# Performance work log

Measured on AMD Instinct MI355X. Metric: run time of the kernel, lower is better.

Reference implementation:

```python
import jax, jax.numpy as jnp
import numpy as np

B, S, D = 2, 2048, 2048
H, DK, DV, LD = 16, 128, 128, 64


def setup_inputs() -> dict:
    key = jax.random.key(0)
    ks = jax.random.split(key, 12)
    s = lambda fan_in: 1.0 / np.sqrt(fan_in)
    return {
        "queries": jax.random.normal(ks[0], (B, S, D), jnp.float32),
        "keys": jax.random.normal(ks[1], (B, S, D), jnp.float32),
        "values": jax.random.normal(ks[2], (B, S, D), jnp.float32),
        # linear_q: Linear(D, DK*H)
        "Wq": jax.random.uniform(ks[3], (D, DK * H), jnp.float32, -s(D), s(D)),
        "bq": jax.random.uniform(ks[4], (DK * H,), jnp.float32, -s(D), s(D)),
        # latent_k_proj / latent_v_proj: Linear(D, LD*H)
        "Wlk": jax.random.uniform(ks[5], (D, LD * H), jnp.float32, -s(D), s(D)),
        "blk": jax.random.uniform(ks[6], (LD * H,), jnp.float32, -s(D), s(D)),
        "Wlv": jax.random.uniform(ks[7], (D, LD * H), jnp.float32, -s(D), s(D)),
        "blv": jax.random.uniform(ks[8], (LD * H,), jnp.float32, -s(D), s(D)),
        # k/v reconstruction: Linear(LD, DK/DV, bias=False), stored [LD, DK]
        "Wkr": jax.random.uniform(ks[9], (LD, DK), jnp.float32, -s(LD), s(LD)),
        "Wvr": jax.random.uniform(ks[10], (LD, DV), jnp.float32, -s(LD), s(LD)),
        # linear_out: Linear(DV*H, D)
        "Wout": jax.random.uniform(ks[11], (DV * H, D), jnp.float32, -s(DV * H), s(DV * H)),
        "bout": jnp.zeros((D,), jnp.float32),
    }


def reference(queries, keys, values, Wq, bq, Wlk, blk, Wlv, blv, Wkr, Wvr, Wout, bout):
    b, sq, _ = queries.shape
    sk = keys.shape[1]
    # Q projection -> [b, H, sq, DK]
    q = (queries @ Wq + bq).reshape(b, sq, H, DK).transpose(0, 2, 1, 3)
    # Low-rank latent K/V -> [b, H, sk, LD]
    lk = (keys @ Wlk + blk).reshape(b, sk, H, LD).transpose(0, 2, 1, 3)
    lv = (values @ Wlv + blv).reshape(b, sk, H, LD).transpose(0, 2, 1, 3)
    # Reconstruct full K/V from latents -> [b, H, sk, DK/DV]
    k = lk @ Wkr
    v = lv @ Wvr
    scores = jnp.einsum('bhqd,bhkd->bhqk', q, k) / np.sqrt(DK).astype(np.float32)
    causal = jnp.triu(jnp.ones((sq, sk), dtype=bool), k=1)
    scores = jnp.where(causal, -jnp.inf, scores)
    attn = jax.nn.softmax(scores, axis=-1)
    out = jnp.einsum('bhqk,bhkd->bhqd', attn, v)  # [b, H, sq, DV]
    out = out.transpose(0, 2, 1, 3).reshape(b, sq, H * DV)
    return out @ Wout + bout
```

## Files before the change

### kernel.cpp

```cpp
#include <hip/hip_runtime.h>

#define S_LEN 2048
#define NH 16

typedef unsigned short u16;
typedef __attribute__((ext_vector_type(8))) short bf16x8;
typedef __attribute__((ext_vector_type(4))) short s16x4;
typedef __attribute__((ext_vector_type(4))) unsigned short u16x4;
typedef __attribute__((ext_vector_type(4))) unsigned int u32x4;
typedef __attribute__((ext_vector_type(4))) float f32x4;

__device__ __forceinline__ u16 f2bf(float f) {
  union { float f; unsigned int i; } x; x.f = f;
  unsigned int r = x.i + 0x7FFFu + ((x.i >> 16) & 1u);
  return (u16)(r >> 16);
}
__device__ __forceinline__ unsigned pk2(float lo, float hi) {
  unsigned r;
  asm("v_cvt_pk_bf16_f32 %0, %1, %2" : "=v"(r) : "v"(lo), "v"(hi));
  return r;
}
__device__ __forceinline__ void glds16(const void* g, void* l) {
  __builtin_amdgcn_global_load_lds((const __attribute__((address_space(1))) void*)g,
                                   (__attribute__((address_space(3))) void*)l, 16, 0, 0);
}

__global__ __launch_bounds__(256) void cast3_f32_bf16(const float* __restrict__ i0,
                                                      const float* __restrict__ i1,
                                                      const float* __restrict__ i2,
                                                      u16* __restrict__ o0,
                                                      u16* __restrict__ o1,
                                                      u16* __restrict__ o2) {
  int z = blockIdx.y;
  const float* in = z == 0 ? i0 : (z == 1 ? i1 : i2);
  u16* out = z == 0 ? o0 : (z == 1 ? o1 : o2);
  size_t i = ((size_t)blockIdx.x * 256 + threadIdx.x) * 8;
  f32x4 a = *(const f32x4*)&in[i];
  f32x4 b = *(const f32x4*)&in[i + 4];
  u32x4 o;
  o[0] = pk2(a[0], a[1]);
  o[1] = pk2(a[2], a[3]);
  o[2] = pk2(b[0], b[1]);
  o[3] = pk2(b[2], b[3]);
  *(u32x4*)&out[i] = o;
}

__global__ __launch_bounds__(256) void cast_f32_bf16(const float* __restrict__ in,
                                                     u16* __restrict__ out) {
  size_t i = ((size_t)blockIdx.x * 256 + threadIdx.x) * 8;
  f32x4 a = *(const f32x4*)&in[i];
  f32x4 b = *(const f32x4*)&in[i + 4];
  u32x4 o;
  o[0] = pk2(a[0], a[1]);
  o[1] = pk2(a[2], a[3]);
  o[2] = pk2(b[0], b[1]);
  o[3] = pk2(b[2], b[3]);
  *(u32x4*)&out[i] = o;
}

__global__ __launch_bounds__(256) void cast2_f32_bf16(const float* __restrict__ i0,
                                                      const float* __restrict__ i1,
                                                      u16* __restrict__ o0,
                                                      u16* __restrict__ o1) {
  const float* in = blockIdx.y ? i1 : i0;
  u16* out = blockIdx.y ? o1 : o0;
  size_t i = ((size_t)blockIdx.x * 256 + threadIdx.x) * 8;
  f32x4 a = *(const f32x4*)&in[i];
  f32x4 b = *(const f32x4*)&in[i + 4];
  u32x4 o;
  o[0] = pk2(a[0], a[1]);
  o[1] = pk2(a[2], a[3]);
  o[2] = pk2(b[0], b[1]);
  o[3] = pk2(b[2], b[3]);
  *(u32x4*)&out[i] = o;
}

__global__ __launch_bounds__(256) void transpose2_f32_bf16(const float* __restrict__ i0,
                                                           const float* __restrict__ i1,
                                                           u16* __restrict__ o0,
                                                           u16* __restrict__ o1,
                                                           int K, int N) {
  const float* in = blockIdx.z ? i1 : i0;
  u16* out = blockIdx.z ? o1 : o0;
  __shared__ u16 tile[64][72];
  int k0 = blockIdx.y * 64, n0 = blockIdx.x * 64;
  int t = threadIdx.x;
#pragma unroll
  for (int i = 0; i < 4; ++i) {
    int idx = i * 256 + t;
    int r = idx >> 4;
    int c4 = (idx & 15) << 2;
    f32x4 v = *(const f32x4*)&in[(size_t)(k0 + r) * N + n0 + c4];
#pragma unroll
    for (int j = 0; j < 4; ++j) tile[r][c4 + j] = f2bf(v[j]);
  }
  __syncthreads();
#pragma unroll
  for (int i = 0; i < 4; ++i) {
    int idx = i * 256 + t;
    int r = idx >> 4;
    int c4 = (idx & 15) << 2;
    u16x4 v;
    v[0] = tile[c4 + 0][r];
    v[1] = tile[c4 + 1][r];
    v[2] = tile[c4 + 2][r];
    v[3] = tile[c4 + 3][r];
    *(u16x4*)&out[(size_t)(n0 + r) * K + k0 + c4] = v;
  }
}

__global__ __launch_bounds__(256) void transpose_f32_bf16(const float* __restrict__ in,
                                                          u16* __restrict__ out,
                                                          int K, int N) {
  __shared__ u16 tile[64][72];
  int k0 = blockIdx.y * 64, n0 = blockIdx.x * 64;
  int t = threadIdx.x;
#pragma unroll
  for (int i = 0; i < 4; ++i) {
    int idx = i * 256 + t;
    int r = idx >> 4;
    int c4 = (idx & 15) << 2;
    f32x4 v = *(const f32x4*)&in[(size_t)(k0 + r) * N + n0 + c4];
#pragma unroll
    for (int j = 0; j < 4; ++j) tile[r][c4 + j] = f2bf(v[j]);
  }
  __syncthreads();
#pragma unroll
  for (int i = 0; i < 4; ++i) {
    int idx = i * 256 + t;
    int r = idx >> 4;
    int c4 = (idx & 15) << 2;
    u16x4 v;
    v[0] = tile[c4 + 0][r];
    v[1] = tile[c4 + 1][r];
    v[2] = tile[c4 + 2][r];
    v[3] = tile[c4 + 3][r];
    *(u16x4*)&out[(size_t)(n0 + r) * K + k0 + c4] = v;
  }
}

__global__ __launch_bounds__(256) void absorb_q(const u16* __restrict__ Wkr,
                                                const u16* __restrict__ Wqb,
                                                u16* __restrict__ Wq2T) {
  int kb = blockIdx.x, h = blockIdx.y;
  int t = threadIdx.x, w = t >> 6, lane = t & 63, lq = lane & 15, hi = lane >> 4;
  int k0 = kb * 128 + w * 32;
  f32x4 acc[4][2];
#pragma unroll
  for (int i = 0; i < 4; ++i)
#pragma unroll
    for (int j = 0; j < 2; ++j) acc[i][j] = (f32x4){0.f, 0.f, 0.f, 0.f};
#pragma unroll
  for (int kk = 0; kk < 4; ++kk) {
    bf16x8 a[4], bb[2];
#pragma unroll
    for (int fld = 0; fld < 4; ++fld)
      a[fld] = *(const bf16x8*)&Wkr[(fld * 16 + lq) * 128 + kk * 32 + hi * 8];
#pragma unroll
    for (int fk = 0; fk < 2; ++fk)
      bb[fk] = *(const bf16x8*)&Wqb[(size_t)(k0 + fk * 16 + lq) * 2048 + h * 128 + kk * 32 + hi * 8];
#pragma unroll
    for (int fld = 0; fld < 4; ++fld)
#pragma unroll
      for (int fk = 0; fk < 2; ++fk)
        acc[fld][fk] = __builtin_amdgcn_mfma_f32_16x16x32_bf16(a[fld], bb[fk], acc[fld][fk], 0, 0, 0);
  }
#pragma unroll
  for (int fld = 0; fld < 4; ++fld)
#pragma unroll
    for (int fk = 0; fk < 2; ++fk)
#pragma unroll
      for (int r = 0; r < 4; ++r)
        Wq2T[(size_t)(h * 64 + fld * 16 + hi * 4 + r) * 2048 + k0 + fk * 16 + lq] =
            f2bf(acc[fld][fk][r]);
}

__global__ __launch_bounds__(256) void absorb_o(const u16* __restrict__ WoutT,
                                                const u16* __restrict__ Wvr,
                                                u16* __restrict__ W2T) {
  int nb = blockIdx.x, h = blockIdx.y;
  int t = threadIdx.x, w = t >> 6, lane = t & 63, lq = lane & 15, hi = lane >> 4;
  int n0 = nb * 128 + w * 32;
  f32x4 acc[2][4];
#pragma unroll
  for (int i = 0; i < 2; ++i)
#pragma unroll
    for (int j = 0; j < 4; ++j) acc[i][j] = (f32x4){0.f, 0.f, 0.f, 0.f};
#pragma unroll
  for (int kk = 0; kk < 4; ++kk) {
    bf16x8 a[2], bb[4];
#pragma unroll
    for (int fn = 0; fn < 2; ++fn)
      a[fn] = *(const bf16x8*)&WoutT[(size_t)(n0 + fn * 16 + lq) * 2048 + h * 128 + kk * 32 + hi * 8];
#pragma unroll
    for (int fld = 0; fld < 4; ++fld)
      bb[fld] = *(const bf16x8*)&Wvr[(fld * 16 + lq) * 128 + kk * 32 + hi * 8];
#pragma unroll
    for (int fn = 0; fn < 2; ++fn)
#pragma unroll
      for (int fld = 0; fld < 4; ++fld)
        acc[fn][fld] = __builtin_amdgcn_mfma_f32_16x16x32_bf16(a[fn], bb[fld], acc[fn][fld], 0, 0, 0);
  }
#pragma unroll
  for (int fn = 0; fn < 2; ++fn)
#pragma unroll
    for (int fld = 0; fld < 4; ++fld)
#pragma unroll
      for (int r = 0; r < 4; ++r)
        W2T[(size_t)(n0 + fn * 16 + hi * 4 + r) * 1024 + h * 64 + fld * 16 + lq] =
            f2bf(acc[fn][fld][r]);
}

__global__ __launch_bounds__(256) void absorb_bq(const float* __restrict__ bq,
                                                 const float* __restrict__ Wkr,
                                                 float* __restrict__ bq2) {
  int n = blockIdx.x * 256 + threadIdx.x;
  int h = n >> 6, ld = n & 63;
  float s = 0.f;
#pragma unroll 8
  for (int dk = 0; dk < 128; ++dk) s += bq[h * 128 + dk] * Wkr[ld * 128 + dk];
  bq2[n] = s;
}

template <bool OF32>
__global__ __launch_bounds__(256, 3) void gemm_dp(const u16* __restrict__ A0,
                                                  const u16* __restrict__ A1,
                                                  const u16* __restrict__ A2,
                                                  const u16* __restrict__ W0,
                                                  const u16* __restrict__ W1,
                                                  const u16* __restrict__ W2,
                                                  const float* __restrict__ b0,
                                                  const float* __restrict__ b1,
                                                  const float* __restrict__ b2,
                                                  void* __restrict__ C0,
                                                  void* __restrict__ C1,
                                                  void* __restrict__ C2,
                                                  int N, int K, int nxl) {
  __shared__ u16 ldsA[3][128 * 32];
  __shared__ u16 ldsB[3][128 * 32];

  int Lb = blockIdx.x;
  int xcd = Lb & 7, slot = Lb >> 3;
  int panel = ((slot >> nxl) << 3) + xcd;
  int x = slot & ((1 << nxl) - 1);
  int z = panel >> 5, y = panel & 31;

  const u16* A = z == 0 ? A0 : (z == 1 ? A1 : A2);
  const u16* Wt = z == 0 ? W0 : (z == 1 ? W1 : W2);
  const float* bias = z == 0 ? b0 : (z == 1 ? b1 : b2);
  void* Cv = z == 0 ? C0 : (z == 1 ? C1 : C2);

  int m0 = y * 128, n0 = x * 128;
  int t = threadIdx.x;
  int lane = t & 63, lq = lane & 15, hi = lane >> 4;
  int w = t >> 6, wm = w >> 1, wn = w & 1;
  int NT = K >> 5;

  auto stage = [&](int q, int kt) {
    u16* lA = &ldsA[q][0];
    u16* lB = &ldsB[q][0];
    int kb = kt * 32;
#pragma unroll
    for (int i = 0; i < 2; ++i) {
      int idx = i * 256 + t;
      int row = idx >> 2, c = idx & 3;
      glds16(&A[(size_t)(m0 + row) * K + kb + ((c ^ ((row >> 1) & 3)) << 3)], lA + idx * 8);
    }
#pragma unroll
    for (int i = 0; i < 2; ++i) {
      int idx = i * 256 + t;
      int row = idx >> 2, c = idx & 3;
      glds16(&Wt[(size_t)(n0 + row) * K + kb + ((c ^ ((row >> 1) & 3)) << 3)], lB + idx * 8);
    }
  };

  f32x4 acc[4][4];
#pragma unroll
  for (int im = 0; im < 4; ++im)
#pragma unroll
    for (int fn = 0; fn < 4; ++fn) acc[im][fn] = (f32x4){0.f, 0.f, 0.f, 0.f};

  stage(0, 0);
  stage(1, 1);
  asm volatile("s_waitcnt vmcnt(4)" ::: "memory");
  __builtin_amdgcn_s_barrier();

  for (int tt = 0; tt < NT; ++tt) {
    int q = tt % 3;
    if (tt + 2 < NT) stage((tt + 2) % 3, tt + 2);
    const u16* lA = &ldsA[q][0];
    const u16* lB = &ldsB[q][0];
    bf16x8 bf[4];
#pragma unroll
    for (int fn = 0; fn < 4; ++fn) {
      int row = wn * 64 + fn * 16 + lq;
      bf[fn] = *(const bf16x8*)&lB[row * 32 + ((hi ^ ((row >> 1) & 3)) << 3)];
    }
    __builtin_amdgcn_s_setprio(1);
#pragma unroll
    for (int im = 0; im < 4; ++im) {
      int row = wm * 64 + im * 16 + lq;
      bf16x8 af = *(const bf16x8*)&lA[row * 32 + ((hi ^ ((row >> 1) & 3)) << 3)];
#pragma unroll
      for (int fn = 0; fn < 4; ++fn)
        acc[im][fn] = __builtin_amdgcn_mfma_f32_16x16x32_bf16(af, bf[fn], acc[im][fn], 0, 0, 0);
    }
    __builtin_amdgcn_s_setprio(0);
    if (tt + 2 < NT)
      asm volatile("s_waitcnt vmcnt(4)" ::: "memory");
    else
      asm volatile("s_waitcnt vmcnt(0)" ::: "memory");
    __builtin_amdgcn_s_barrier();
  }

#pragma unroll
  for (int im = 0; im < 4; ++im)
#pragma unroll
    for (int fn = 0; fn < 4; ++fn) {
      int col = n0 + wn * 64 + fn * 16 + lq;
      float bv = bias[col];
      int rbase = m0 + wm * 64 + im * 16 + hi * 4;
#pragma unroll
      for (int r = 0; r < 4; ++r) {
        float v = acc[im][fn][r] + bv;
        if constexpr (OF32)
          ((float*)Cv)[(size_t)(rbase + r) * N + col] = v;
        else
          ((u16*)Cv)[(size_t)(rbase + r) * N + col] = f2bf(v);
      }
    }
}

__global__ __launch_bounds__(256) void transpose_lv(const u16* __restrict__ LV,
                                                    u16* __restrict__ out) {
  __shared__ u16 tile[64 * 72];
  int st = blockIdx.x, bh = blockIdx.y;
  int b = bh >> 4, h = bh & 15;
  int t = threadIdx.x;
  int s0 = st * 64;
#pragma unroll
  for (int i = 0; i < 2; ++i) {
    int idx = i * 256 + t;
    int sr = idx >> 3, c8 = idx & 7;
    bf16x8 v = *(const bf16x8*)&LV[(size_t)(b * S_LEN + s0 + sr) * 1024 + h * 64 + c8 * 8];
    int pos = (sr & 32) + ((sr & 12) << 1) + ((sr & 16) >> 2) + (sr & 3);
#pragma unroll
    for (int j = 0; j < 8; ++j) tile[(c8 * 8 + j) * 72 + pos] = (u16)v[j];
  }
  __syncthreads();
  u16* ob = out + (size_t)bh * 64 * S_LEN;
#pragma unroll
  for (int i = 0; i < 2; ++i) {
    int idx = i * 256 + t;
    int ld = idx >> 3, c8 = idx & 7;
    bf16x8 v = *(const bf16x8*)&tile[ld * 72 + c8 * 8];
    *(bf16x8*)&ob[(size_t)ld * S_LEN + s0 + c8 * 8] = v;
  }
}

__global__ __launch_bounds__(256) void mla_attn5(const u16* __restrict__ Qp,
                                                 const u16* __restrict__ LK,
                                                 const u16* __restrict__ LVt,
                                                 u16* __restrict__ O) {
  __shared__ u16 smem[16384];
  int Lb = blockIdx.x + blockIdx.y * 8;
  int half = Lb >> 9;
  int i0 = Lb & 511;
  int xcd = i0 & 7, ii = i0 >> 3;
  int bh = xcd * 4 + (ii & 3);
  int pr = ii >> 2;
  int qsup = half ? (31 - pr) : pr;
  int b = bh >> 4, h = bh & 15;
  int t = threadIdx.x, w = t >> 6, lane = t & 63, lq = lane & 15, hi = lane >> 4;
  int lq7 = lq & 7;

  const u16* Kb = LK + (size_t)b * S_LEN * 1024 + h * 64;
  const u16* Vb = LVt + (size_t)bh * 64 * S_LEN;
  const float scale = 0.08838834764831845f;

  auto stage = [&](int buf, int k0) {
    u16* lK = smem + buf * 4096;
    u16* lV = smem + 8192 + buf * 4096;
#pragma unroll
    for (int i = 0; i < 2; ++i) {
      int idx = i * 256 + t;
      int row = idx >> 3, c8 = idx & 7;
      glds16(Kb + (size_t)(k0 + row) * 1024 + ((c8 ^ (row & 7)) << 3), lK + idx * 8);
    }
#pragma unroll
    for (int i = 0; i < 2; ++i) {
      int idx = i * 256 + t;
      int row = idx >> 3, c8 = idx & 7;
      glds16(Vb + (size_t)row * S_LEN + k0 + ((c8 ^ (row & 7)) << 3), lV + idx * 8);
    }
  };

  int qb = qsup * 64;
  int nt = qsup + 1;
  int q0 = qb + w * 16;
  int kmax = q0 + 16;

  bf16x8 qf[2];
  {
    const u16* Qrow = Qp + (size_t)(b * S_LEN + q0 + lq) * 1024 + h * 64;
    qf[0] = *(const bf16x8*)&Qrow[hi * 8];
    qf[1] = *(const bf16x8*)&Qrow[32 + hi * 8];
  }

  f32x4 acc[4];
#pragma unroll
  for (int f = 0; f < 4; ++f) acc[f] = (f32x4){0.f, 0.f, 0.f, 0.f};
  float m = -1e30f, l = 0.f;

  stage(0, 0);
  __syncthreads();
  for (int tt = 0; tt < nt; ++tt) {
    int cur = tt & 1;
    if (tt + 1 < nt) stage(cur ^ 1, (tt + 1) * 64);
    int k0 = tt * 64;
    if (k0 < kmax) {
      const u16* lK = smem + cur * 4096;
      const u16* lV = smem + 8192 + cur * 4096;
      f32x4 sc[4];
#pragma unroll
      for (int kf = 0; kf < 4; ++kf) sc[kf] = (f32x4){0.f, 0.f, 0.f, 0.f};
      __builtin_amdgcn_s_setprio(1);
#pragma unroll
      for (int kf = 0; kf < 4; ++kf) {
        const u16* kr = lK + (kf * 16 + lq) * 64;
#pragma unroll
        for (int d0 = 0; d0 < 2; ++d0) {
          bf16x8 af = *(const bf16x8*)&kr[(((d0 << 2) + hi) ^ lq7) << 3];
          sc[kf] = __builtin_amdgcn_mfma_f32_16x16x32_bf16(af, qf[d0], sc[kf], 0, 0, 0);
        }
      }
      __builtin_amdgcn_s_setprio(0);
      int q = q0 + lq;
      float sv[16];
#pragma unroll
      for (int kf = 0; kf < 4; ++kf)
#pragma unroll
        for (int r = 0; r < 4; ++r) sv[kf * 4 + r] = sc[kf][r] * scale;
      if (k0 + 63 > q0) {
#pragma unroll
        for (int kf = 0; kf < 4; ++kf)
#pragma unroll
          for (int r = 0; r < 4; ++r)
            if (k0 + kf * 16 + hi * 4 + r > q) sv[kf * 4 + r] = -1e30f;
      }
      float tm = sv[0];
#pragma unroll
      for (int j = 1; j < 16; ++j) tm = fmaxf(tm, sv[j]);
      tm = fmaxf(tm, __shfl_xor(tm, 16));
      tm = fmaxf(tm, __shfl_xor(tm, 32));
      float p[16], ps = 0.f;
      if (__all(tm <= m + 8.f)) {
#pragma unroll
        for (int j = 0; j < 16; ++j) { p[j] = __expf(sv[j] - m); ps += p[j]; }
        ps += __shfl_xor(ps, 16);
        ps += __shfl_xor(ps, 32);
        l += ps;
      } else {
        float mnew = fmaxf(m, tm);
        float alpha = __expf(m - mnew);
#pragma unroll
        for (int j = 0; j < 16; ++j) { p[j] = __expf(sv[j] - mnew); ps += p[j]; }
        ps += __shfl_xor(ps, 16);
        ps += __shfl_xor(ps, 32);
        l = l * alpha + ps;
        m = mnew;
#pragma unroll
        for (int f = 0; f < 4; ++f) {
          acc[f][0] *= alpha; acc[f][1] *= alpha;
          acc[f][2] *= alpha; acc[f][3] *= alpha;
        }
      }
      bf16x8 pb[2];
#pragma unroll
      for (int ks = 0; ks < 2; ++ks) {
        union { u32x4 u; bf16x8 v; } pu;
#pragma unroll
        for (int wd = 0; wd < 4; ++wd) pu.u[wd] = pk2(p[ks * 8 + 2 * wd], p[ks * 8 + 2 * wd + 1]);
        pb[ks] = pu.v;
      }
      __builtin_amdgcn_s_setprio(1);
#pragma unroll
      for (int f = 0; f < 4; ++f) {
        const u16* vr = lV + (f * 16 + lq) * 64;
#pragma unroll
        for (int ks = 0; ks < 2; ++ks) {
          bf16x8 va = *(const bf16x8*)&vr[(((ks << 2) + hi) ^ lq7) << 3];
          acc[f] = __builtin_amdgcn_mfma_f32_16x16x32_bf16(va, pb[ks], acc[f], 0, 0, 0);
        }
      }
      __builtin_amdgcn_s_setprio(0);
    }
    __syncthreads();
  }
  {
    float inv = 1.f / l;
    int qloc = w * 16 + lq;
#pragma unroll
    for (int f = 0; f < 4; ++f)
#pragma unroll
      for (int r = 0; r < 4; ++r) {
        int col = f * 16 + hi * 4 + r;
        smem[qloc * 64 + (((col >> 3) ^ lq7) << 3) + (col & 7)] = f2bf(acc[f][r] * inv);
      }
  }
  __syncthreads();
#pragma unroll
  for (int i = 0; i < 2; ++i) {
    int cid = i * 256 + t;
    int q = cid >> 3, ch = cid & 7;
    bf16x8 v = *(const bf16x8*)&smem[q * 64 + ((ch ^ (q & 7)) << 3)];
    *(bf16x8*)&O[(size_t)(b * S_LEN + qb + q) * 1024 + h * 64 + (ch << 3)] = v;
  }
}

extern "C" void kernel_launch(void* const* d_in, const int* in_sizes, int n_in,
                              void* d_out, int out_size, void* d_ws, size_t ws_size,
                              hipStream_t stream) {
  const float* queries = (const float*)d_in[0];
  const float* keys    = (const float*)d_in[1];
  const float* values  = (const float*)d_in[2];
  const float* Wq      = (const float*)d_in[3];
  const float* bq      = (const float*)d_in[4];
  const float* Wlk     = (const float*)d_in[5];
  const float* blk     = (const float*)d_in[6];
  const float* Wlv     = (const float*)d_in[7];
  const float* blv     = (const float*)d_in[8];
  const float* Wkr     = (const float*)d_in[9];
  const float* Wvr     = (const float*)d_in[10];
  const float* Wout    = (const float*)d_in[11];
  const float* bout    = (const float*)d_in[12];

  u16* ws = (u16*)d_ws;
  u16* WqBf  = ws; ws += (size_t)2048 * 2048;
  u16* WkrBf = ws; ws += 64 * 128;
  u16* WvrBf = ws; ws += 64 * 128;
  u16* WoutT = ws; ws += (size_t)2048 * 2048;
  u16* WlkT  = ws; ws += (size_t)1024 * 2048;
  u16* WlvT  = ws; ws += (size_t)1024 * 2048;
  u16* Wq2T  = ws; ws += (size_t)1024 * 2048;
  u16* W2T   = ws; ws += (size_t)2048 * 1024;
  float* bq2 = (float*)ws; ws += 2048;
  u16* Qin   = ws; ws += (size_t)4096 * 2048;
  u16* Kin   = ws; ws += (size_t)4096 * 2048;
  u16* Vin   = ws; ws += (size_t)4096 * 2048;
  u16* Qp    = ws; ws += (size_t)4096 * 1024;
  u16* LKb   = ws; ws += (size_t)4096 * 1024;
  u16* LVb   = ws; ws += (size_t)4096 * 1024;
  u16* LVt = Kin;
  u16* Ob  = Qin;

  dim3 blk256(256);
  cast3_f32_bf16<<<dim3(4096, 3), blk256, 0, stream>>>(queries, keys, values, Qin, Kin, Vin);
  cast_f32_bf16<<<dim3(2048), blk256, 0, stream>>>(Wq, WqBf);
  cast2_f32_bf16<<<dim3(4, 2), blk256, 0, stream>>>(Wkr, Wvr, WkrBf, WvrBf);

  transpose2_f32_bf16<<<dim3(16, 32, 2), blk256, 0, stream>>>(Wlk, Wlv, WlkT, WlvT, 2048, 1024);
  transpose_f32_bf16<<<dim3(32, 32), blk256, 0, stream>>>(Wout, WoutT, 2048, 2048);

  absorb_q<<<dim3(16, 16), blk256, 0, stream>>>(WkrBf, WqBf, Wq2T);
  absorb_o<<<dim3(16, 16), blk256, 0, stream>>>(WoutT, WvrBf, W2T);
  absorb_bq<<<dim3(4), blk256, 0, stream>>>(bq, Wkr, bq2);

  gemm_dp<false><<<dim3(768), blk256, 0, stream>>>(
      Qin, Kin, Vin, Wq2T, WlkT, WlvT, bq2, blk, blv, Qp, LKb, LVb, 1024, 2048, 3);

  transpose_lv<<<dim3(32, 32), blk256, 0, stream>>>(LVb, LVt);

  mla_attn5<<<dim3(8, 128), blk256, 0, stream>>>(Qp, LKb, LVt, Ob);

  gemm_dp<true><<<dim3(512), blk256, 0, stream>>>(
      Ob, Ob, Ob, W2T, W2T, W2T, bout, bout, bout, d_out, d_out, d_out, 2048, 1024, 4);
}
```

Before: 203.4 us.

## Fuse fp32-to-bf16 activation cast into projection GEMM A-tile loading

Drops the separate cast kernel for queries/keys/values. The projection GEMM now reads fp32 activations straight into registers, converts them to bf16 and writes them to LDS, with a new two-slot register pipeline for A alongside async LDS loads for B. This removes a full write and re-read of three 4096x2048 bf16 intermediates. In exchange the GEMM fetches twice the A bytes from global memory, the pipeline carries more register pressure, and the waitcnt scheduling is more complex.

```diff
diff --git a/kernel.cpp b/kernel.cpp
--- a/kernel.cpp
+++ b/kernel.cpp
@@ -23,26 +23,6 @@
 __device__ __forceinline__ void glds16(const void* g, void* l) {
   __builtin_amdgcn_global_load_lds((const __attribute__((address_space(1))) void*)g,
                                    (__attribute__((address_space(3))) void*)l, 16, 0, 0);
-}
-
-__global__ __launch_bounds__(256) void cast3_f32_bf16(const float* __restrict__ i0,
-                                                      const float* __restrict__ i1,
-                                                      const float* __restrict__ i2,
-                                                      u16* __restrict__ o0,
-                                                      u16* __restrict__ o1,
-                                                      u16* __restrict__ o2) {
-  int z = blockIdx.y;
-  const float* in = z == 0 ? i0 : (z == 1 ? i1 : i2);
-  u16* out = z == 0 ? o0 : (z == 1 ? o1 : o2);
-  size_t i = ((size_t)blockIdx.x * 256 + threadIdx.x) * 8;
-  f32x4 a = *(const f32x4*)&in[i];
-  f32x4 b = *(const f32x4*)&in[i + 4];
-  u32x4 o;
-  o[0] = pk2(a[0], a[1]);
-  o[1] = pk2(a[2], a[3]);
-  o[2] = pk2(b[0], b[1]);
-  o[3] = pk2(b[2], b[3]);
-  *(u32x4*)&out[i] = o;
 }
 
 __global__ __launch_bounds__(256) void cast_f32_bf16(const float* __restrict__ in,
@@ -222,22 +202,21 @@
   bq2[n] = s;
 }
 
-template <bool OF32>
-__global__ __launch_bounds__(256, 3) void gemm_dp(const u16* __restrict__ A0,
-                                                  const u16* __restrict__ A1,
-                                                  const u16* __restrict__ A2,
-                                                  const u16* __restrict__ W0,
-                                                  const u16* __restrict__ W1,
-                                                  const u16* __restrict__ W2,
-                                                  const float* __restrict__ b0,
-                                                  const float* __restrict__ b1,
-                                                  const float* __restrict__ b2,
-                                                  void* __restrict__ C0,
-                                                  void* __restrict__ C1,
-                                                  void* __restrict__ C2,
-                                                  int N, int K, int nxl) {
-  __shared__ u16 ldsA[3][128 * 32];
-  __shared__ u16 ldsB[3][128 * 32];
+__global__ __launch_bounds__(256, 3) void gemm_projf(const float* __restrict__ A0,
+                                                     const float* __restrict__ A1,
+                                                     const float* __restrict__ A2,
+                                                     const u16* __restrict__ W0,
+                                                     const u16* __restrict__ W1,
+                                                     const u16* __restrict__ W2,
+                                                     const float* __restrict__ b0,
+                                                     const float* __restrict__ b1,
+                                                     const float* __restrict__ b2,
+                                                     u16* __restrict__ C0,
+                                                     u16* __restrict__ C1,
+                                                     u16* __restrict__ C2) {
+  const int N = 1024, K = 2048, nxl = 3, NT = 64;
+  __shared__ u16 abuf[2][128 * 32];
+  __shared__ u16 bbuf[3][128 * 32];
 
   int Lb = blockIdx.x;
   int xcd = Lb & 7, slot = Lb >> 3;
@@ -245,10 +224,146 @@
   int x = slot & ((1 << nxl) - 1);
   int z = panel >> 5, y = panel & 31;
 
-  const u16* A = z == 0 ? A0 : (z == 1 ? A1 : A2);
+  const float* A = z == 0 ? A0 : (z == 1 ? A1 : A2);
   const u16* Wt = z == 0 ? W0 : (z == 1 ? W1 : W2);
   const float* bias = z == 0 ? b0 : (z == 1 ? b1 : b2);
-  void* Cv = z == 0 ? C0 : (z == 1 ? C1 : C2);
+  u16* C = z == 0 ? C0 : (z == 1 ? C1 : C2);
+
+  int m0 = y * 128, n0 = x * 128;
+  int t = threadIdx.x;
+  int lane = t & 63, lq = lane & 15, hi = lane >> 4;
+  int w = t >> 6, wm = w >> 1, wn = w & 1;
+
+  struct a16 { f32x4 lo, hi; };
+  a16 areg[2][2];
+
+  f32x4 acc[4][4];
+#pragma unroll
+  for (int im = 0; im < 4; ++im)
+#pragma unroll
+    for (int fn = 0; fn < 4; ++fn) acc[im][fn] = (f32x4){0.f, 0.f, 0.f, 0.f};
+
+#define LOADA(SLOT, KT)                                                              \
+  do {                                                                               \
+    int kb_ = (KT) * 32;                                                             \
+    _Pragma("unroll") for (int i = 0; i < 2; ++i) {                                  \
+      int idx = i * 256 + t, row = idx >> 2, c = idx & 3;                            \
+      const float* ap = &A[(size_t)(m0 + row) * K + kb_ + ((c ^ ((row >> 1) & 3)) << 3)]; \
+      areg[SLOT][i].lo = *(const f32x4*)ap;                                          \
+      areg[SLOT][i].hi = *(const f32x4*)(ap + 4);                                    \
+    }                                                                                \
+  } while (0)
+
+#define WRITEA(SLOT)                                                                 \
+  do {                                                                               \
+    _Pragma("unroll") for (int i = 0; i < 2; ++i) {                                  \
+      u32x4 o;                                                                       \
+      o[0] = pk2(areg[SLOT][i].lo[0], areg[SLOT][i].lo[1]);                          \
+      o[1] = pk2(areg[SLOT][i].lo[2], areg[SLOT][i].lo[3]);                          \
+      o[2] = pk2(areg[SLOT][i].hi[0], areg[SLOT][i].hi[1]);                          \
+      o[3] = pk2(areg[SLOT][i].hi[2], areg[SLOT][i].hi[3]);                          \
+      *(u32x4*)&abuf[SLOT][(i * 256 + t) * 8] = o;                                   \
+    }                                                                                \
+  } while (0)
+
+#define STAGEB(KT)                                                                   \
+  do {                                                                               \
+    int kb_ = (KT) * 32;                                                             \
+    u16* lB_ = &bbuf[(KT) % 3][0];                                                   \
+    _Pragma("unroll") for (int i = 0; i < 2; ++i) {                                  \
+      int idx = i * 256 + t, row = idx >> 2, c = idx & 3;                            \
+      glds16(&Wt[(size_t)(n0 + row) * K + kb_ + ((c ^ ((row >> 1) & 3)) << 3)], lB_ + idx * 8); \
+    }                                                                                \
+  } while (0)
+
+#define COMPUTE(PAR, TT)                                                             \
+  do {                                                                               \
+    const u16* lB_ = &bbuf[(TT) % 3][0];                                             \
+    bf16x8 bf[4];                                                                    \
+    _Pragma("unroll") for (int fn = 0; fn < 4; ++fn) {                               \
+      int row = wn * 64 + fn * 16 + lq;                                              \
+      bf[fn] = *(const bf16x8*)&lB_[row * 32 + ((hi ^ ((row >> 1) & 3)) << 3)];      \
+    }                                                                                \
+    __builtin_amdgcn_s_setprio(1);                                                   \
+    _Pragma("unroll") for (int im = 0; im < 4; ++im) {                               \
+      int row = wm * 64 + im * 16 + lq;                                              \
+      bf16x8 af = *(const bf16x8*)&abuf[PAR][row * 32 + ((hi ^ ((row >> 1) & 3)) << 3)]; \
+      _Pragma("unroll") for (int fn = 0; fn < 4; ++fn)                               \
+        acc[im][fn] = __builtin_amdgcn_mfma_f32_16x16x32_bf16(af, bf[fn], acc[im][fn], 0, 0, 0); \
+    }                                                                                \
+    __builtin_amdgcn_s_setprio(0);                                                   \
+  } while (0)
+
+#define PSTEP(TT, PAR)                                                               \
+  do {                                                                               \
+    if ((TT) + 1 < NT) {                                                             \
+      asm volatile("s_waitcnt vmcnt(2)" ::: "memory");                               \
+      WRITEA(PAR ^ 1);                                                               \
+    }                                                                                \
+    __builtin_amdgcn_sched_barrier(0);                                               \
+    if ((TT) + 2 < NT) LOADA(PAR, (TT) + 2);                                         \
+    __builtin_amdgcn_sched_barrier(0);                                               \
+    if ((TT) + 2 < NT) STAGEB((TT) + 2);                                             \
+    __builtin_amdgcn_sched_barrier(0);                                               \
+    COMPUTE(PAR, TT);                                                                \
+    if ((TT) + 2 < NT)                                                               \
+      asm volatile("s_waitcnt vmcnt(6)" ::: "memory");                               \
+    else                                                                             \
+      asm volatile("s_waitcnt vmcnt(0)" ::: "memory");                               \
+    asm volatile("s_waitcnt lgkmcnt(0)" ::: "memory");                               \
+    __builtin_amdgcn_s_barrier();                                                    \
+  } while (0)
+
+  LOADA(0, 0);
+  __builtin_amdgcn_sched_barrier(0);
+  STAGEB(0);
+  __builtin_amdgcn_sched_barrier(0);
+  LOADA(1, 1);
+  __builtin_amdgcn_sched_barrier(0);
+  STAGEB(1);
+  __builtin_amdgcn_sched_barrier(0);
+  asm volatile("s_waitcnt vmcnt(8)" ::: "memory");
+  WRITEA(0);
+  asm volatile("s_waitcnt vmcnt(6)" ::: "memory");
+  asm volatile("s_waitcnt lgkmcnt(0)" ::: "memory");
+  __builtin_amdgcn_s_barrier();
+
+  for (int tt = 0; tt < NT; tt += 2) {
+    PSTEP(tt, 0);
+    PSTEP(tt + 1, 1);
+  }
+
+#pragma unroll
+  for (int im = 0; im < 4; ++im)
+#pragma unroll
+    for (int fn = 0; fn < 4; ++fn) {
+      int col = n0 + wn * 64 + fn * 16 + lq;
+      float bv = bias[col];
+      int rbase = m0 + wm * 64 + im * 16 + hi * 4;
+#pragma unroll
+      for (int r = 0; r < 4; ++r)
+        C[(size_t)(rbase + r) * N + col] = f2bf(acc[im][fn][r] + bv);
+    }
+#undef LOADA
+#undef WRITEA
+#undef STAGEB
+#undef COMPUTE
+#undef PSTEP
+}
+
+__global__ __launch_bounds__(256, 3) void gemm_dp(const u16* __restrict__ A,
+                                                  const u16* __restrict__ Wt,
+                                                  const float* __restrict__ bias,
+                                                  float* __restrict__ Cv,
+                                                  int N, int K, int nxl) {
+  __shared__ u16 ldsA[3][128 * 32];
+  __shared__ u16 ldsB[3][128 * 32];
+
+  int Lb = blockIdx.x;
+  int xcd = Lb & 7, slot = Lb >> 3;
+  int panel = ((slot >> nxl) << 3) + xcd;
+  int x = slot & ((1 << nxl) - 1);
+  int y = panel & 31;
 
   int m0 = y * 128, n0 = x * 128;
   int t = threadIdx.x;
@@ -321,13 +436,8 @@
       float bv = bias[col];
       int rbase = m0 + wm * 64 + im * 16 + hi * 4;
 #pragma unroll
-      for (int r = 0; r < 4; ++r) {
-        float v = acc[im][fn][r] + bv;
-        if constexpr (OF32)
-          ((float*)Cv)[(size_t)(rbase + r) * N + col] = v;
-        else
-          ((u16*)Cv)[(size_t)(rbase + r) * N + col] = f2bf(v);
-      }
+      for (int r = 0; r < 4; ++r)
+        Cv[(size_t)(rbase + r) * N + col] = acc[im][fn][r] + bv;
     }
 }
 
@@ -545,17 +655,13 @@
   u16* Wq2T  = ws; ws += (size_t)1024 * 2048;
   u16* W2T   = ws; ws += (size_t)2048 * 1024;
   float* bq2 = (float*)ws; ws += 2048;
-  u16* Qin   = ws; ws += (size_t)4096 * 2048;
-  u16* Kin   = ws; ws += (size_t)4096 * 2048;
-  u16* Vin   = ws; ws += (size_t)4096 * 2048;
   u16* Qp    = ws; ws += (size_t)4096 * 1024;
   u16* LKb   = ws; ws += (size_t)4096 * 1024;
   u16* LVb   = ws; ws += (size_t)4096 * 1024;
-  u16* LVt = Kin;
-  u16* Ob  = Qin;
+  u16* LVt   = ws; ws += (size_t)32 * 64 * S_LEN;
+  u16* Ob    = ws; ws += (size_t)4096 * 1024;
 
   dim3 blk256(256);
-  cast3_f32_bf16<<<dim3(4096, 3), blk256, 0, stream>>>(queries, keys, values, Qin, Kin, Vin);
   cast_f32_bf16<<<dim3(2048), blk256, 0, stream>>>(Wq, WqBf);
   cast2_f32_bf16<<<dim3(4, 2), blk256, 0, stream>>>(Wkr, Wvr, WkrBf, WvrBf);
 
@@ -566,13 +672,13 @@
   absorb_o<<<dim3(16, 16), blk256, 0, stream>>>(WoutT, WvrBf, W2T);
   absorb_bq<<<dim3(4), blk256, 0, stream>>>(bq, Wkr, bq2);
 
-  gemm_dp<false><<<dim3(768), blk256, 0, stream>>>(
-      Qin, Kin, Vin, Wq2T, WlkT, WlvT, bq2, blk, blv, Qp, LKb, LVb, 1024, 2048, 3);
+  gemm_projf<<<dim3(768), blk256, 0, stream>>>(
+      queries, keys, values, Wq2T, WlkT, WlvT, bq2, blk, blv, Qp, LKb, LVb);
 
   transpose_lv<<<dim3(32, 32), blk256, 0, stream>>>(LVb, LVt);
 
   mla_attn5<<<dim3(8, 128), blk256, 0, stream>>>(Qp, LKb, LVt, Ob);
 
-  gemm_dp<true><<<dim3(512), blk256, 0, stream>>>(
-      Ob, Ob, Ob, W2T, W2T, W2T, bout, bout, bout, d_out, d_out, d_out, 2048, 1024, 4);
-}
+  gemm_dp<<<dim3(512), blk256, 0, stream>>>(
+      Ob, W2T, bout, (float*)d_out, 2048, 1024, 4);
+}
```

After: 189.6 us (median of 2 runs). -6.8%, faster.
